# Kernel tuning notes

Measured on AMD Instinct MI355X. Metric: run time of the kernel, lower is better.

The kernel has to match this reference:

```python
import jax, jax.numpy as jnp
import numpy as np
from jax import lax

GAMMA = 1.0   # soft-min temperature (init kwarg)
BIG = 1e10    # finite stand-in for +inf (safe gradients, exp(-BIG/gamma) == 0 in fp32)


def _pairwise_sqdist(X, Z):
    # X: (N, T, d), Z: (T, d) -> D: (N, T, T) squared Euclidean, without (N,T,T,d) intermediate
    x2 = jnp.sum(X * X, axis=-1)              # (N, T)
    z2 = jnp.sum(Z * Z, axis=-1)              # (T,)
    xz = jnp.einsum('ntd,sd->nts', X, Z)      # (N, T, T)
    return x2[:, :, None] + z2[None, None, :] - 2.0 * xz


def _softdtw_batch(D, gamma):
    # D: (N, T, T) cost matrices. Anti-diagonal wavefront DP:
    #   R[i,j] = D[i,j] + softmin(R[i-1,j], R[i,j-1], R[i-1,j-1]),  R[0,0]=0, borders=BIG
    # Diagonal k = i + j (i,j in 1..T); diagonal arrays indexed by ii = i-1 in [0, T).
    N, T, _ = D.shape
    ii = jnp.arange(T)
    inv_g = 1.0 / gamma

    def softmin(a, b, c):
        s = jnp.stack([a, b, c], axis=0) * (-inv_g)
        return -gamma * jax.scipy.special.logsumexp(s, axis=0)

    def step(carry, k):
        d_prev2, d_prev1 = carry              # diagonals k-2 and k-1, each (N, T)
        jj = k - 2 - ii                        # column index j-1 for row index ii
        valid = (jj >= 0) & (jj < T)
        dvals = jnp.take_along_axis(
            D, jnp.clip(jj, 0, T - 1)[None, :, None], axis=2)[..., 0]  # (N, T)
        r_left = d_prev1                                   # R[i, j-1]
        r_up = jnp.concatenate(
            [jnp.full((N, 1), BIG, D.dtype), d_prev1[:, :-1]], axis=1)  # R[i-1, j]
        corner = jnp.where(k == 2, jnp.asarray(0.0, D.dtype), jnp.asarray(BIG, D.dtype))
        r_diag = jnp.concatenate(
            [jnp.broadcast_to(corner, (N, 1)), d_prev2[:, :-1]], axis=1)  # R[i-1, j-1]
        new_d = jnp.where(valid[None, :], dvals + softmin(r_up, r_left, r_diag),
                          jnp.asarray(BIG, D.dtype))
        return (d_prev1, new_d), None

    d0 = jnp.full((N, T), BIG, D.dtype)
    (_, last), _ = lax.scan(step, (d0, d0), jnp.arange(2, 2 * T + 1))
    return last[:, T - 1]                      # R[T, T] per sample


def setup_inputs() -> dict:
    key = jax.random.key(0)
    k1, k2, k3 = jax.random.split(key, 3)
    N, T, d = 64, 512, 16
    X = jax.random.normal(k1, (N, T, d), dtype=jnp.float32)
    weights = jax.random.uniform(k2, (N,), dtype=jnp.float32)
    Z = jax.random.normal(k3, (T, d), dtype=jnp.float32)
    return {"X": X, "weights": weights, "Z": Z}


def reference(X, weights, Z):
    D = _pairwise_sqdist(X, Z)                 # (N, T, T)
    sdtw = _softdtw_batch(D, GAMMA)            # (N,)
    return jnp.sum(weights * sdtw)             # scalar barycenter loss
```

## Files before the change

### kernel.cpp

```cpp
#include <hip/hip_runtime.h>

#define TT 512
#define BIGS 1.4426950408889634e10f
#define LOG2E 1.4426950408889634f
#define M2L  (-2.0f * 1.4426950408889634f)
#define LN2F 0.69314718055994531f
#define P_SS 16
#define G_LAG 96
#define N_SS 54
#define RSTR 130

typedef _Float16 h2 __attribute__((ext_vector_type(2)));

__device__ __forceinline__ unsigned pk(float a, float b) {
    h2 v; v.x = (_Float16)a; v.y = (_Float16)b;
    return __builtin_bit_cast(unsigned, v);
}

#if __has_builtin(__builtin_amdgcn_fdot2)
#define FDOT2(a, b, c) __builtin_amdgcn_fdot2(__builtin_bit_cast(h2, (a)), \
                                              __builtin_bit_cast(h2, (b)), (c), false)
#else
__device__ __forceinline__ float fdot2_sw(unsigned a, unsigned b, float c) {
    h2 ha = __builtin_bit_cast(h2, a), hb = __builtin_bit_cast(h2, b);
    return c + (float)ha.x * (float)hb.x + (float)ha.y * (float)hb.y;
}
#define FDOT2(a, b, c) fdot2_sw((a), (b), (c))
#endif

#if __has_builtin(__builtin_amdgcn_exp2f)
#define EXP2F(x) __builtin_amdgcn_exp2f(x)
#else
#define EXP2F(x) exp2f(x)
#endif

#define ZROW(jv) (((((jv) & 1)) << 8) | ((((jv) >> 1)) & 255))

__device__ __forceinline__ float dppshr1(float x, float old) {
#if __has_builtin(__builtin_amdgcn_update_dpp)
    return __builtin_bit_cast(float,
        __builtin_amdgcn_update_dpp(__builtin_bit_cast(int, old),
                                    __builtin_bit_cast(int, x),
                                    0x138 , 0xF, 0xF, false));
#else
    const float v = __shfl_up(x, 1);
    return ((threadIdx.x & 63) == 0) ? old : v;
#endif
}

__global__ __launch_bounds__(512, 1) void k_fused(const float* __restrict__ X,
                                                  const float* __restrict__ Z,
                                                  const float* __restrict__ w,
                                                  float* __restrict__ out) {
    const int tt = threadIdx.x;
    const int t  = tt & 63;
    const int wv = tt >> 6;
    const int bd = (wv < 4) ? wv : (wv - 4);
    const int n  = blockIdx.x;

    __shared__ uint4    ZA[2][512];
    __shared__ float    Zs2p[512];
    __shared__ float2   seam[4][64];
    __shared__ unsigned ring[4][64][RSTR];

    {
        const int r = tt;
        const float4* zp = (const float4*)(Z + (size_t)r * 16);
        const float4 a0 = zp[0], a1 = zp[1], a2 = zp[2], a3 = zp[3];
        float sv = 0.0f;
        sv = fmaf(a0.x, a0.x, sv); sv = fmaf(a0.y, a0.y, sv);
        sv = fmaf(a0.z, a0.z, sv); sv = fmaf(a0.w, a0.w, sv);
        sv = fmaf(a1.x, a1.x, sv); sv = fmaf(a1.y, a1.y, sv);
        sv = fmaf(a1.z, a1.z, sv); sv = fmaf(a1.w, a1.w, sv);
        sv = fmaf(a2.x, a2.x, sv); sv = fmaf(a2.y, a2.y, sv);
        sv = fmaf(a2.z, a2.z, sv); sv = fmaf(a2.w, a2.w, sv);
        sv = fmaf(a3.x, a3.x, sv); sv = fmaf(a3.y, a3.y, sv);
        sv = fmaf(a3.z, a3.z, sv); sv = fmaf(a3.w, a3.w, sv);
        const int idx = ((r & 1) << 8) | (r >> 1);
        ZA[0][idx] = make_uint4(pk(a0.x, a0.y), pk(a0.z, a0.w),
                                pk(a1.x, a1.y), pk(a1.z, a1.w));
        ZA[1][idx] = make_uint4(pk(a2.x, a2.y), pk(a2.z, a2.w),
                                pk(a3.x, a3.y), pk(a3.z, a3.w));
        Zs2p[idx] = LOG2E * sv;
    }
    if (tt < 256) ((float2*)&seam[0][0])[tt] = make_float2(BIGS, 1.0f);

    const int i0 = 128 * bd + 2 * t;
    unsigned Xu[2][8];
    float    xs2[2];
    const float* xp = X + ((size_t)n * TT + i0) * 16;
#pragma unroll
    for (int q = 0; q < 2; ++q) {
        const float4* xr = (const float4*)(xp + q * 16);
        const float4 a0 = xr[0], a1 = xr[1], a2 = xr[2], a3 = xr[3];
        float sv = 0.0f;
        sv = fmaf(a0.x, a0.x, sv); sv = fmaf(a0.y, a0.y, sv);
        sv = fmaf(a0.z, a0.z, sv); sv = fmaf(a0.w, a0.w, sv);
        sv = fmaf(a1.x, a1.x, sv); sv = fmaf(a1.y, a1.y, sv);
        sv = fmaf(a1.z, a1.z, sv); sv = fmaf(a1.w, a1.w, sv);
        sv = fmaf(a2.x, a2.x, sv); sv = fmaf(a2.y, a2.y, sv);
        sv = fmaf(a2.z, a2.z, sv); sv = fmaf(a2.w, a2.w, sv);
        sv = fmaf(a3.x, a3.x, sv); sv = fmaf(a3.y, a3.y, sv);
        sv = fmaf(a3.z, a3.z, sv); sv = fmaf(a3.w, a3.w, sv);
        xs2[q] = LOG2E * sv;
        Xu[q][0] = pk(a0.x, a0.y); Xu[q][1] = pk(a0.z, a0.w);
        Xu[q][2] = pk(a1.x, a1.y); Xu[q][3] = pk(a1.z, a1.w);
        Xu[q][4] = pk(a2.x, a2.y); Xu[q][5] = pk(a2.z, a2.w);
        Xu[q][6] = pk(a3.x, a3.y); Xu[q][7] = pk(a3.z, a3.w);
    }
    const float wgt = w[n];
    const float2* rKS = &seam[bd][0];
    unsigned* const rg = &ring[bd][t][0];
    __syncthreads();

#define PRODUCE(Tv)                                                           \
    {                                                                         \
        const int base_ = (Tv) << 4;                                          \
        const int wb_ = base_ & 127;                                          \
        _Pragma("unroll 4")                                                   \
        for (int cc = 0; cc < 16; ++cc) {                                     \
            const int zr = ZROW(base_ + cc);                \
            const uint4 z0 = ZA[0][zr], z1 = ZA[1][zr];                       \
            const float zz = Zs2p[zr];                                        \
            float a0 = 0.0f, b0 = 0.0f, a1 = 0.0f, b1 = 0.0f;                 \
            a0 = FDOT2(z0.x, Xu[0][0], a0); a0 = FDOT2(z0.y, Xu[0][1], a0);   \
            a0 = FDOT2(z0.z, Xu[0][2], a0); a0 = FDOT2(z0.w, Xu[0][3], a0);   \
            b0 = FDOT2(z1.x, Xu[0][4], b0); b0 = FDOT2(z1.y, Xu[0][5], b0);   \
            b0 = FDOT2(z1.z, Xu[0][6], b0); b0 = FDOT2(z1.w, Xu[0][7], b0);   \
            a1 = FDOT2(z0.x, Xu[1][0], a1); a1 = FDOT2(z0.y, Xu[1][1], a1);   \
            a1 = FDOT2(z0.z, Xu[1][2], a1); a1 = FDOT2(z0.w, Xu[1][3], a1);   \
            b1 = FDOT2(z1.x, Xu[1][4], b1); b1 = FDOT2(z1.y, Xu[1][5], b1);   \
            b1 = FDOT2(z1.z, Xu[1][6], b1); b1 = FDOT2(z1.w, Xu[1][7], b1);   \
            const float dd0 = fmaf(M2L, a0 + b0, xs2[0] + zz);                \
            const float dd1 = fmaf(M2L, a1 + b1, xs2[1] + zz);                \
            rg[wb_ + cc] = pk(dd0, dd1);                                      \
        }                                                                     \
    }

    if (wv >= 4 && bd == 0) { PRODUCE(0) PRODUCE(1) }
    __syncthreads();

    float RpK[2], RpS[2], poK, poS, bnK, bnS;
    float2 smv[2];
    unsigned rv[2];
    RpK[0] = RpK[1] = BIGS; RpS[0] = RpS[1] = 1.0f;
    poK = BIGS; poS = 1.0f; bnK = BIGS; bnS = 1.0f;
    smv[0] = smv[1] = make_float2(BIGS, 1.0f);
    rv[0] = rv[1] = 0u;

#define TICK(q, tl)                                                           \
    {                                                                         \
        const float unK = bnK, unS = bnS;                                     \
        const float2 sprev = smv[q];                     \
        smv[q] = rKS[((tl) + 3) & 63];                     \
        const h2 dh = __builtin_bit_cast(h2, rv[q]);                          \
        rv[q] = rg[((unsigned)((tl) + 2 - t)) & 127];      \
        const float dd0 = (float)dh.x;                                        \
        const float dd1 = (float)dh.y;                                        \
        const float l0K = RpK[0], l0S = RpS[0];                               \
        const float m0 = fminf(fminf(unK, l0K), poK);                         \
        const float s0 = EXP2F(m0 - unK) * unS                                \
                       + EXP2F(m0 - l0K) * l0S                                \
                       + EXP2F(m0 - poK) * poS;                               \
        const float K0 = dd0 + m0;                                            \
        const float l1K = RpK[1], l1S = RpS[1];                               \
        const float m1 = fminf(fminf(K0, l1K), l0K);                          \
        const float s1 = EXP2F(m1 - K0) * s0                                  \
                       + EXP2F(m1 - l1K) * l1S                                \
                       + EXP2F(m1 - l0K) * l0S;                               \
        const float K1 = dd1 + m1;                                            \
        const int j = (tl) - t;                                               \
        const bool ok = (j >= 0) && (j < 512);                                \
        RpK[0] = ok ? K0 : RpK[0];  RpS[0] = ok ? s0 : RpS[0];                \
        RpK[1] = ok ? K1 : RpK[1];  RpS[1] = ok ? s1 : RpS[1];                \
        if (ok && bd < 3 && t == 63) {                                        \
            seam[bd + 1][j & 63] = make_float2(RpK[1], RpS[1]);               \
        }                                                                     \
        poK = unK; poS = unS;                                                 \
        bnK = dppshr1(RpK[1], sprev.x);           \
        bnS = dppshr1(RpS[1], sprev.y);                                       \
    }

#define RENORM                                                                \
    {                                                                         \
        _Pragma("unroll")                                                     \
        for (int q = 0; q < 2; ++q) {                                         \
            const int e = (int)(__float_as_uint(RpS[q]) >> 23) - 127;         \
            RpS[q] = __uint_as_float(__float_as_uint(RpS[q])                  \
                                     - ((unsigned)e << 23));                  \
            RpK[q] -= (float)e;                                               \
        }                                                                     \
    }

#pragma unroll 1
    for (int s = 0; s < N_SS; ++s) {
        if (wv >= 4) {
            const int T = s - 6 * bd + 2;
            if (T >= 0 && T <= 31) PRODUCE(T)
        } else {
            const int tb = P_SS * s - G_LAG * bd;
            if (tb >= 0 && tb <= 574) {
                if (tb == 0) {
                    RpK[0] = RpK[1] = BIGS; RpS[0] = RpS[1] = 1.0f;
                    poK = (bd == 0 && t == 0) ? 0.0f : BIGS; poS = 1.0f;
                    const float2 r0 = rKS[0];
                    bnK = r0.x; bnS = r0.y;
                    smv[1] = rKS[1];
                    smv[0] = rKS[2];
                    rv[0] = rg[((unsigned)(0 - t)) & 127];
                    rv[1] = rg[((unsigned)(1 - t)) & 127];
                }
                TICK(0, tb + 0)  TICK(1, tb + 1)  TICK(0, tb + 2)  TICK(1, tb + 3)
                TICK(0, tb + 4)  TICK(1, tb + 5)  TICK(0, tb + 6)  TICK(1, tb + 7)
                RENORM
                TICK(0, tb + 8)  TICK(1, tb + 9)  TICK(0, tb + 10) TICK(1, tb + 11)
                TICK(0, tb + 12) TICK(1, tb + 13) TICK(0, tb + 14) TICK(1, tb + 15)
                RENORM
            }
        }
        __syncthreads();
    }
#undef TICK
#undef RENORM
#undef PRODUCE

    if (wv == 3 && t == 63) {
        atomicAdd(out, wgt * (RpK[1] - log2f(RpS[1])) * LN2F);
    }
}

__global__ void k_zero(float* out) {
    if (threadIdx.x == 0) out[0] = 0.0f;
}

extern "C" void kernel_launch(void* const* d_in, const int* in_sizes, int n_in,
                              void* d_out, int out_size, void* d_ws, size_t ws_size,
                              hipStream_t stream) {
    const float* X = (const float*)d_in[0];
    const float* w = (const float*)d_in[1];
    const float* Z = (const float*)d_in[2];
    float* out = (float*)d_out;

    hipLaunchKernelGGL(k_zero, dim3(1), dim3(64), 0, stream, out);
    hipLaunchKernelGGL(k_fused, dim3(64), dim3(512), 0, stream, X, Z, w, out);
}
```

Before: 178.7 us.

## Specialize interior super-steps, raise consumer wave priority, shrink stage lag

Interior super-steps, where every lane's column index is in range, now run a TICK variant with the bounds check compiled out. Consumer waves raise their scheduling priority around the DP body. The seam values are now loaded directly from LDS inside each tick, replacing the prefetched ring of two. The inter-wave lag drops from 96 to 80 and the producer offset from 6 to 5 per band, which shortens the loop from 54 to 51 super-steps. The tighter lag assumes seam data still arrives in time, and the direct LDS load puts its latency back on the critical dependency chain.

After: 171.8 us. 1.04x faster.

```diff
diff --git a/kernel.cpp b/kernel.cpp
--- a/kernel.cpp
+++ b/kernel.cpp
@@ -6,8 +6,8 @@
 #define M2L  (-2.0f * 1.4426950408889634f)
 #define LN2F 0.69314718055994531f
 #define P_SS 16
-#define G_LAG 96
-#define N_SS 54
+#define G_LAG 80
+#define N_SS 51
 #define RSTR 130
 
 typedef _Float16 h2 __attribute__((ext_vector_type(2)));
@@ -141,18 +141,15 @@
     __syncthreads();
 
     float RpK[2], RpS[2], poK, poS, bnK, bnS;
-    float2 smv[2];
     unsigned rv[2];
     RpK[0] = RpK[1] = BIGS; RpS[0] = RpS[1] = 1.0f;
     poK = BIGS; poS = 1.0f; bnK = BIGS; bnS = 1.0f;
-    smv[0] = smv[1] = make_float2(BIGS, 1.0f);
     rv[0] = rv[1] = 0u;
 
-#define TICK(q, tl)                                                           \
+#define TICK(q, tl, ALLOK)                                                    \
     {                                                                         \
+        const float2 sprev = rKS[((tl) + 1) & 63];        \
         const float unK = bnK, unS = bnS;                                     \
-        const float2 sprev = smv[q];                     \
-        smv[q] = rKS[((tl) + 3) & 63];                     \
         const h2 dh = __builtin_bit_cast(h2, rv[q]);                          \
         rv[q] = rg[((unsigned)((tl) + 2 - t)) & 127];      \
         const float dd0 = (float)dh.x;                                        \
@@ -170,7 +167,7 @@
                        + EXP2F(m1 - l0K) * l0S;                               \
         const float K1 = dd1 + m1;                                            \
         const int j = (tl) - t;                                               \
-        const bool ok = (j >= 0) && (j < 512);                                \
+        const bool ok = (ALLOK) ? true : ((j >= 0) && (j < 512));             \
         RpK[0] = ok ? K0 : RpK[0];  RpS[0] = ok ? s0 : RpS[0];                \
         RpK[1] = ok ? K1 : RpK[1];  RpS[1] = ok ? s1 : RpS[1];                \
         if (ok && bd < 3 && t == 63) {                                        \
@@ -192,36 +189,46 @@
         }                                                                     \
     }
 
+#define SS_BODY(A)                                                            \
+    TICK(0, tb + 0, A)  TICK(1, tb + 1, A)  TICK(0, tb + 2, A)                \
+    TICK(1, tb + 3, A)  TICK(0, tb + 4, A)  TICK(1, tb + 5, A)                \
+    TICK(0, tb + 6, A)  TICK(1, tb + 7, A)                                    \
+    RENORM                                                                    \
+    TICK(0, tb + 8, A)  TICK(1, tb + 9, A)  TICK(0, tb + 10, A)               \
+    TICK(1, tb + 11, A) TICK(0, tb + 12, A) TICK(1, tb + 13, A)               \
+    TICK(0, tb + 14, A) TICK(1, tb + 15, A)                                   \
+    RENORM
+
 #pragma unroll 1
     for (int s = 0; s < N_SS; ++s) {
         if (wv >= 4) {
-            const int T = s - 6 * bd + 2;
+            const int T = s - 5 * bd + 2;
             if (T >= 0 && T <= 31) PRODUCE(T)
         } else {
             const int tb = P_SS * s - G_LAG * bd;
-            if (tb >= 0 && tb <= 574) {
+            if (tb >= 64 && tb <= 496) {
+                __builtin_amdgcn_s_setprio(1);
+                SS_BODY(1)
+                __builtin_amdgcn_s_setprio(0);
+            } else if (tb >= 0 && tb <= 574) {
                 if (tb == 0) {
                     RpK[0] = RpK[1] = BIGS; RpS[0] = RpS[1] = 1.0f;
                     poK = (bd == 0 && t == 0) ? 0.0f : BIGS; poS = 1.0f;
                     const float2 r0 = rKS[0];
                     bnK = r0.x; bnS = r0.y;
-                    smv[1] = rKS[1];
-                    smv[0] = rKS[2];
                     rv[0] = rg[((unsigned)(0 - t)) & 127];
                     rv[1] = rg[((unsigned)(1 - t)) & 127];
                 }
-                TICK(0, tb + 0)  TICK(1, tb + 1)  TICK(0, tb + 2)  TICK(1, tb + 3)
-                TICK(0, tb + 4)  TICK(1, tb + 5)  TICK(0, tb + 6)  TICK(1, tb + 7)
-                RENORM
-                TICK(0, tb + 8)  TICK(1, tb + 9)  TICK(0, tb + 10) TICK(1, tb + 11)
-                TICK(0, tb + 12) TICK(1, tb + 13) TICK(0, tb + 14) TICK(1, tb + 15)
-                RENORM
+                __builtin_amdgcn_s_setprio(1);
+                SS_BODY(0)
+                __builtin_amdgcn_s_setprio(0);
             }
         }
         __syncthreads();
     }
 #undef TICK
 #undef RENORM
+#undef SS_BODY
 #undef PRODUCE
 
     if (wv == 3 && t == 63) {
```
